# Kernel optimization log

Measured on AMD Instinct MI355X. Metric: run time of the kernel, lower is better.

## Reference

```python
import jax, jax.numpy as jnp
import numpy as np

DIM = 1024
NUM_HEADS = 16
HEAD_DIM = DIM // NUM_HEADS
SCALE = HEAD_DIM ** -0.5


def setup_inputs() -> dict:
    key = jax.random.key(0)
    k_x, k_wqkv, k_bqkv, k_wp, k_bp = jax.random.split(key, 5)
    B, C, D = 4, 1024, DIM
    x = jax.random.normal(k_x, (B, C, D), dtype=jnp.float32)
    # nn.Linear stores weight as (out, in); we keep (in, out) for x @ W
    w_qkv = jax.random.normal(k_wqkv, (D, 3 * D), dtype=jnp.float32) * (D ** -0.5)
    b_qkv = jax.random.normal(k_bqkv, (3 * D,), dtype=jnp.float32) * 0.02
    w_proj = jax.random.normal(k_wp, (D, D), dtype=jnp.float32) * (D ** -0.5)
    b_proj = jax.random.normal(k_bp, (D,), dtype=jnp.float32) * 0.02
    return {"x": x, "w_qkv": w_qkv, "b_qkv": b_qkv, "w_proj": w_proj, "b_proj": b_proj}


def reference(x, w_qkv, b_qkv, w_proj, b_proj):
    B, C, D = x.shape
    H, Hd = NUM_HEADS, HEAD_DIM
    qkv = x @ w_qkv + b_qkv                       # (B, C, 3D)
    qkv = qkv.reshape(B, C, 3, H, Hd)
    q = qkv[:, :, 0].transpose(0, 2, 1, 3)        # (B, H, C, Hd)
    k = qkv[:, :, 1].transpose(0, 2, 1, 3)
    v = qkv[:, :, 2].transpose(0, 2, 1, 3)
    attn = jnp.einsum('bhqd,bhkd->bhqk', q, k) * SCALE
    attn = jax.nn.softmax(attn, axis=-1)
    out = jnp.einsum('bhqk,bhkd->bhqd', attn, v)  # (B, H, C, Hd)
    out = out.transpose(0, 2, 1, 3).reshape(B, C, D)
    return out @ w_proj + b_proj
```

## Files before the change

### kernel.cpp

```cpp
#include <hip/hip_runtime.h>
#include <cstdint>

#define BB 4
#define CC 1024
#define DD 1024
#define HH 16
#define HD 64
#define NH3 3072

typedef __attribute__((ext_vector_type(8))) short short8;
typedef __attribute__((ext_vector_type(4))) float f32x4;

#define MFMA16(a, b, c) __builtin_amdgcn_mfma_f32_16x16x32_bf16(a, b, c, 0, 0, 0)
#define EXP2 __builtin_amdgcn_exp2f

__device__ __forceinline__ void glds16(const void* g, void* l) {
    __builtin_amdgcn_global_load_lds(
        (const __attribute__((address_space(1))) void*)g,
        (__attribute__((address_space(3))) void*)l, 16, 0, 0);
}

__device__ __forceinline__ ushort f2bf(float f) {
    union { float f; uint32_t u; } v; v.f = f;
    uint32_t r = v.u + 0x7FFF + ((v.u >> 16) & 1);
    return (ushort)(r >> 16);
}

__device__ __forceinline__ uint32_t pack2bf(float a, float b) {
    uint32_t ua = __float_as_uint(a), ub = __float_as_uint(b);
    ua += 0x7FFF + ((ua >> 16) & 1);
    ub += 0x7FFF + ((ub >> 16) & 1);
    return __builtin_amdgcn_perm(ua, ub, 0x03020706);
}

__global__ __launch_bounds__(256)
void prep_kernel(const float* __restrict__ x, ushort* __restrict__ xbf,
                 const float* __restrict__ wqkv, ushort* __restrict__ wqkvT,
                 const float* __restrict__ wprj, ushort* __restrict__ wprjT)
{
    __shared__ float Ts[64 * 65];
    const int blk = blockIdx.x;
    const int t = threadIdx.x;

    if (blk < 4096) {
        int i = blk * 256 + t;
        float4 v = ((const float4*)x)[i];
        ushort4 o;
        o.x = f2bf(v.x); o.y = f2bf(v.y); o.z = f2bf(v.z); o.w = f2bf(v.w);
        ((ushort4*)xbf)[i] = o;
        return;
    }

    const float* in; ushort* outp; int K, N, n0, k0;
    if (blk < 4864) {
        int bx = blk - 4096;
        in = wqkv; outp = wqkvT; K = DD; N = NH3;
        n0 = (bx % 48) * 64; k0 = (bx / 48) * 64;
    } else {
        int bx = blk - 4864;
        in = wprj; outp = wprjT; K = DD; N = DD;
        n0 = (bx % 16) * 64; k0 = (bx / 16) * 64;
    }
    #pragma unroll
    for (int i = 0; i < 16; ++i) {
        int idx = t + i * 256;
        int r = idx >> 6, c = idx & 63;
        Ts[r * 65 + c] = in[(size_t)(k0 + r) * N + n0 + c];
    }
    __syncthreads();
    #pragma unroll
    for (int i = 0; i < 16; ++i) {
        int idx = t + i * 256;
        int rr = idx >> 6, cc = idx & 63;
        outp[(size_t)(n0 + rr) * K + k0 + cc] = f2bf(Ts[cc * 65 + rr]);
    }
}

template<int MODE, int MT>
__global__ __launch_bounds__(256)
void gemm_bt(const ushort* __restrict__ A, const ushort* __restrict__ Bt,
             const float* __restrict__ bias, float* __restrict__ Cf,
             ushort* __restrict__ qb, ushort* __restrict__ kb, ushort* __restrict__ vtb,
             int M, int N, int K)
{
    constexpr int MI = MT / 32;
    __shared__ ushort As[2][MT * 32];
    __shared__ ushort Bs[2][128 * 32];

    const int tid = threadIdx.x;
    const int wid = tid >> 6, lane = tid & 63;
    const int quad = lane >> 4, l15 = lane & 15;
    const int m0 = blockIdx.y * MT, n0 = blockIdx.x * 128;
    const int wm = (wid >> 1) * (MT / 2), wn = (wid & 1) * 64;

    const int sr = lane >> 2;
    const int sc = lane & 3;

    const int ar0 = wid * (MT / 4) + sr;
    const int acg0 = sc ^ ((ar0 >> 1) & 3);
    const int acg1 = sc ^ (((ar0 + 16) >> 1) & 3);
    const ushort* Ar0 = A + (size_t)(m0 + ar0) * K + acg0 * 8;
    const ushort* Ar1 = A + (size_t)(m0 + ar0 + 16) * K + acg1 * 8;
    const int br0 = wid * 32 + sr;
    const int bcg0 = sc ^ ((br0 >> 1) & 3);
    const int bcg1 = sc ^ (((br0 + 16) >> 1) & 3);
    const ushort* Br0 = Bt + (size_t)(n0 + br0) * K + bcg0 * 8;
    const ushort* Br1 = Bt + (size_t)(n0 + br0 + 16) * K + bcg1 * 8;

    f32x4 acc[MI][4];
    #pragma unroll
    for (int i = 0; i < MI; ++i)
        #pragma unroll
        for (int j = 0; j < 4; ++j) acc[i][j] = (f32x4)(0.0f);

    glds16(Ar0, &As[0][(wid * (MT / 4)) * 32]);
    glds16(Br0, &Bs[0][(wid * 32) * 32]);
    if (MT == 128) glds16(Ar1, &As[0][(wid * 32 + 16) * 32]);
    glds16(Br1, &Bs[0][(wid * 32 + 16) * 32]);

    int buf = 0;
    for (int k0 = 0; k0 < K; k0 += 32) {
        __syncthreads();
        if (k0 + 32 < K) {
            const int kn = k0 + 32;
            glds16(Ar0 + kn, &As[buf ^ 1][(wid * (MT / 4)) * 32]);
            glds16(Br0 + kn, &Bs[buf ^ 1][(wid * 32) * 32]);
            if (MT == 128) glds16(Ar1 + kn, &As[buf ^ 1][(wid * 32 + 16) * 32]);
            glds16(Br1 + kn, &Bs[buf ^ 1][(wid * 32 + 16) * 32]);
        }

        short8 af[MI], bf[4];
        #pragma unroll
        for (int i = 0; i < MI; ++i) {
            int row = wm + i * 16 + l15;
            af[i] = *(const short8*)(&As[buf][row * 32 + (quad ^ ((row >> 1) & 3)) * 8]);
        }
        #pragma unroll
        for (int j = 0; j < 4; ++j) {
            int col = wn + j * 16 + l15;
            bf[j] = *(const short8*)(&Bs[buf][col * 32 + (quad ^ ((col >> 1) & 3)) * 8]);
        }
        #pragma unroll
        for (int i = 0; i < MI; ++i)
            #pragma unroll
            for (int j = 0; j < 4; ++j)
                acc[i][j] = MFMA16(af[i], bf[j], acc[i][j]);
        buf ^= 1;
    }

    if (MODE == 0) {
        #pragma unroll
        for (int i = 0; i < MI; ++i) {
            int row = m0 + wm + i * 16 + quad * 4;
            #pragma unroll
            for (int j = 0; j < 4; ++j) {
                int col = n0 + wn + j * 16 + l15;
                float bv = bias[col];
                #pragma unroll
                for (int r = 0; r < 4; ++r)
                    Cf[(size_t)(row + r) * N + col] = acc[i][j][r] + bv;
            }
        }
    } else {
        #pragma unroll
        for (int j = 0; j < 4; ++j) {
            int n = n0 + wn + j * 16 + l15;
            int three = n >> 10;
            int h = (n >> 6) & 15;
            int hd = n & 63;
            float scale = (three == 0) ? 0.1803368801f : 1.0f;
            float bv = bias[n];
            #pragma unroll
            for (int i = 0; i < MI; ++i) {
                int row = m0 + wm + i * 16 + quad * 4;
                #pragma unroll
                for (int r = 0; r < 4; ++r) {
                    int m = row + r;
                    int b = m >> 10, c = m & 1023;
                    ushort val = f2bf((acc[i][j][r] + bv) * scale);
                    if (three == 0)
                        qb[((size_t)((b * HH + h) * CC) + c) * HD + hd] = val;
                    else if (three == 1)
                        kb[((size_t)((b * HH + h) * CC) + c) * HD + hd] = val;
                    else
                        vtb[((size_t)((b * HH + h) * HD) + hd) * CC + c] = val;
                }
            }
        }
    }
}

__global__ __launch_bounds__(256)
void attn_mfma6(const ushort* __restrict__ qb, const ushort* __restrict__ kb,
                const ushort* __restrict__ vt, ushort* __restrict__ attnb)
{
    __shared__ ushort lds[2 * 4096 + 3 * 4096 + 2 * 9216];
    const uint K0 = 0, K1 = 4096;
    const uint V0 = 8192, V1 = 12288, V2 = 16384;
    const uint P0 = 20480, P1 = 29696;

    const int tid = threadIdx.x;
    const int wid = tid >> 6, lane = tid & 63;
    const int quad = lane >> 4, l15 = lane & 15;
    const int bh = blockIdx.x & 63;
    const int qt = blockIdx.x >> 6;
    const int q0 = qt * 128;
    const int b = bh >> 4, h = bh & 15;

    const ushort* Qp  = qb + ((size_t)bh * CC + q0) * HD;
    const ushort* Kp  = kb + (size_t)bh * CC * HD;
    const ushort* Vtp = vt + (size_t)bh * HD * CC;

    const int sr = lane >> 3;
    const int sc = lane & 7;

    short8 qf[2][2];
    #pragma unroll
    for (int q2 = 0; q2 < 2; ++q2) {
        int row = wid * 32 + q2 * 16 + l15;
        #pragma unroll
        for (int s = 0; s < 2; ++s)
            qf[q2][s] = *(const short8*)(Qp + (size_t)row * HD + (s * 4 + quad) * 8);
    }

    const int kr = wid * 16 + sr;
    const int cgA = sc ^ (kr & 7);
    const int cgB = sc ^ ((kr + 8) & 7);
    const ushort* Kr0 = Kp  + (size_t)kr * HD + cgA * 8;
    const ushort* Kr1 = Kp  + (size_t)(kr + 8) * HD + cgB * 8;
    const ushort* Vr0 = Vtp + (size_t)kr * CC + cgA * 8;
    const ushort* Vr1 = Vtp + (size_t)(kr + 8) * CC + cgB * 8;

    const uint stg0 = (wid * 16) * 64;
    const uint stg1 = (wid * 16 + 8) * 64;

    glds16(Kr0, lds + K0 + stg0);
    glds16(Kr1, lds + K0 + stg1);
    glds16(Vr0, lds + V0 + stg0);
    glds16(Vr1, lds + V0 + stg1);

    f32x4 oacc[2][4];
    #pragma unroll
    for (int q2 = 0; q2 < 2; ++q2)
        #pragma unroll
        for (int hb = 0; hb < 4; ++hb) oacc[q2][hb] = (f32x4)(0.0f);
    float lsum[2] = {0.0f, 0.0f};

    uint ksC = K0, ksN = K1;
    uint vsP = V2, vsC = V0, vsN = V1;
    uint psC = P0, psP = P1;

    for (int kt = 0; kt < 16; ++kt) {
        __syncthreads();
        if (kt < 15) {
            const int koff = (kt + 1) * 64;
            glds16(Kr0 + (size_t)koff * HD, lds + ksN + stg0);
            glds16(Kr1 + (size_t)koff * HD, lds + ksN + stg1);
            glds16(Vr0 + koff,              lds + vsN + stg0);
            glds16(Vr1 + koff,              lds + vsN + stg1);
        }

        if (kt > 0) {
            short8 vf[4][2];
            #pragma unroll
            for (int hb = 0; hb < 4; ++hb) {
                int hr = hb * 16 + l15;
                vf[hb][0] = *(const short8*)(lds + vsP + hr * 64 + ((quad ^ (hr & 7)) * 8));
                vf[hb][1] = *(const short8*)(lds + vsP + hr * 64 + (((4 + quad) ^ (hr & 7)) * 8));
            }
            #pragma unroll
            for (int q2 = 0; q2 < 2; ++q2) {
                int row = wid * 32 + q2 * 16 + l15;
                short8 pf0 = *(const short8*)(lds + psP + row * 72 + quad * 8);
                short8 pf1 = *(const short8*)(lds + psP + row * 72 + 32 + quad * 8);
                #pragma unroll
                for (int hb = 0; hb < 4; ++hb) {
                    oacc[q2][hb] = MFMA16(pf0, vf[hb][0], oacc[q2][hb]);
                    oacc[q2][hb] = MFMA16(pf1, vf[hb][1], oacc[q2][hb]);
                }
            }
        }

        #pragma unroll
        for (int kb2 = 0; kb2 < 4; ++kb2) {
            int krow = kb2 * 16 + l15;
            short8 kf0 = *(const short8*)(lds + ksC + krow * 64 + ((quad ^ (krow & 7)) * 8));
            short8 kf1 = *(const short8*)(lds + ksC + krow * 64 + (((4 + quad) ^ (krow & 7)) * 8));
            #pragma unroll
            for (int q2 = 0; q2 < 2; ++q2) {
                f32x4 st = (f32x4)(0.0f);
                st = MFMA16(kf0, qf[q2][0], st);
                st = MFMA16(kf1, qf[q2][1], st);
                float p0 = EXP2(st[0]);
                float p1 = EXP2(st[1]);
                float p2 = EXP2(st[2]);
                float p3 = EXP2(st[3]);
                lsum[q2] += (p0 + p1) + (p2 + p3);
                int row = wid * 32 + q2 * 16 + l15;
                *(uint2*)(lds + psC + row * 72 + kb2 * 16 + quad * 4) =
                    make_uint2(pack2bf(p0, p1), pack2bf(p2, p3));
            }
        }

        uint t = vsP; vsP = vsC; vsC = vsN; vsN = t;
        t = ksC; ksC = ksN; ksN = t;
        t = psP; psP = psC; psC = t;
    }

    {
        short8 vf[4][2];
        #pragma unroll
        for (int hb = 0; hb < 4; ++hb) {
            int hr = hb * 16 + l15;
            vf[hb][0] = *(const short8*)(lds + vsP + hr * 64 + ((quad ^ (hr & 7)) * 8));
            vf[hb][1] = *(const short8*)(lds + vsP + hr * 64 + (((4 + quad) ^ (hr & 7)) * 8));
        }
        #pragma unroll
        for (int q2 = 0; q2 < 2; ++q2) {
            int row = wid * 32 + q2 * 16 + l15;
            short8 pf0 = *(const short8*)(lds + psP + row * 72 + quad * 8);
            short8 pf1 = *(const short8*)(lds + psP + row * 72 + 32 + quad * 8);
            #pragma unroll
            for (int hb = 0; hb < 4; ++hb) {
                oacc[q2][hb] = MFMA16(pf0, vf[hb][0], oacc[q2][hb]);
                oacc[q2][hb] = MFMA16(pf1, vf[hb][1], oacc[q2][hb]);
            }
        }
    }

    #pragma unroll
    for (int q2 = 0; q2 < 2; ++q2) {
        lsum[q2] += __shfl_xor(lsum[q2], 16);
        lsum[q2] += __shfl_xor(lsum[q2], 32);
    }

    #pragma unroll
    for (int q2 = 0; q2 < 2; ++q2) {
        #pragma unroll
        for (int r = 0; r < 4; ++r) {
            float inv = 1.0f / __shfl(lsum[q2], (lane & 48) | (quad * 4 + r));
            int c = q0 + wid * 32 + q2 * 16 + quad * 4 + r;
            #pragma unroll
            for (int hb = 0; hb < 4; ++hb) {
                int d = h * 64 + hb * 16 + l15;
                attnb[((size_t)(b * CC + c)) * DD + d] = f2bf(oacc[q2][hb][r] * inv);
            }
        }
    }
}

extern "C" void kernel_launch(void* const* d_in, const int* in_sizes, int n_in,
                              void* d_out, int out_size, void* d_ws, size_t ws_size,
                              hipStream_t stream)
{
    (void)in_sizes; (void)n_in; (void)out_size; (void)ws_size;
    const float* x      = (const float*)d_in[0];
    const float* w_qkv  = (const float*)d_in[1];
    const float* b_qkv  = (const float*)d_in[2];
    const float* w_proj = (const float*)d_in[3];
    const float* b_proj = (const float*)d_in[4];
    float* out = (float*)d_out;

    ushort* p = (ushort*)d_ws;
    ushort* xbf   = p;  p += (size_t)4 * 1024 * 1024;
    ushort* wqkvT = p;  p += (size_t)3 * 1024 * 1024;
    ushort* wprjT = p;  p += (size_t)1 * 1024 * 1024;
    ushort* qbuf  = p;  p += (size_t)4 * 1024 * 1024;
    ushort* kbuf  = p;  p += (size_t)4 * 1024 * 1024;
    ushort* vtb   = p;  p += (size_t)4 * 1024 * 1024;
    ushort* attnb = p;  p += (size_t)4 * 1024 * 1024;

    prep_kernel<<<5120, 256, 0, stream>>>(x, xbf, w_qkv, wqkvT, w_proj, wprjT);

    gemm_bt<1, 128><<<dim3(NH3 / 128, (BB * CC) / 128), 256, 0, stream>>>(
        xbf, wqkvT, b_qkv, nullptr, qbuf, kbuf, vtb, BB * CC, NH3, DD);

    attn_mfma6<<<512, 256, 0, stream>>>(qbuf, kbuf, vtb, attnb);

    gemm_bt<0, 64><<<dim3(DD / 128, (BB * CC) / 64), 256, 0, stream>>>(
        attnb, wprjT, b_proj, out, nullptr, nullptr, nullptr, BB * CC, DD, DD);
}
```

Baseline: 177.8 us.

## Add 256x256 tiled QKV GEMM with 4-stage LDS pipeline

Replaces the 128x128 QKV projection GEMM with a dedicated kernel that uses 256x256 block tiles, 512 threads and a four-buffer direct global-to-LDS pipeline with swizzled layout. The larger tiles are meant to raise operand reuse and cut global and LDS traffic per MFMA. The trade-off is a grid of only 192 blocks, which leaves some CUs idle, plus higher register and LDS use per block.

```diff
diff --git a/kernel.cpp b/kernel.cpp
--- a/kernel.cpp
+++ b/kernel.cpp
@@ -190,6 +190,108 @@
     }
 }
 
+__global__ __launch_bounds__(512, 2)
+void gemm_qkv256(const ushort* __restrict__ A, const ushort* __restrict__ Bt,
+                 const float* __restrict__ bias,
+                 ushort* __restrict__ qb, ushort* __restrict__ kb,
+                 ushort* __restrict__ vtb)
+{
+    constexpr int K  = DD;
+    constexpr int KT = K / 32;
+    __shared__ ushort lds[4][16384];
+
+    const int tid = threadIdx.x;
+    const int wid = tid >> 6, lane = tid & 63;
+    const int quad = lane >> 4, l15 = lane & 15;
+    const int m0 = blockIdx.y * 256, n0 = blockIdx.x * 256;
+    const int wm = (wid >> 2) * 128, wn = (wid & 3) * 64;
+
+    const int sr = lane >> 2, sc = lane & 3;
+    const int ra = wid * 16 + sr;
+    const int cga = sc ^ ((ra >> 1) & 3);
+    const ushort* Ap0 = A  + (size_t)(m0 + ra) * K + cga * 8;
+    const ushort* Ap1 = Ap0 + (size_t)128 * K;
+    const ushort* Bp0 = Bt + (size_t)(n0 + ra) * K + cga * 8;
+    const ushort* Bp1 = Bp0 + (size_t)128 * K;
+    const int sA0 = (wid * 16) * 32;
+    const int sA1 = sA0 + 128 * 32;
+    const int sB0 = 8192 + sA0;
+    const int sB1 = 8192 + sA1;
+
+#define QSTAGE(kt) do { ushort* lb_ = &lds[(kt) & 3][0]; const int ko_ = (kt) * 32; \
+        glds16(Ap0 + ko_, lb_ + sA0); \
+        glds16(Ap1 + ko_, lb_ + sA1); \
+        glds16(Bp0 + ko_, lb_ + sB0); \
+        glds16(Bp1 + ko_, lb_ + sB1); } while (0)
+
+    f32x4 acc[8][4];
+    #pragma unroll
+    for (int i = 0; i < 8; ++i)
+        #pragma unroll
+        for (int j = 0; j < 4; ++j) acc[i][j] = (f32x4)(0.0f);
+
+    QSTAGE(0); QSTAGE(1); QSTAGE(2);
+
+#define QPHASE(kt, VMS, DOSTAGE) do { \
+        asm volatile("s_waitcnt " VMS "\n\ts_barrier" ::: "memory"); \
+        const ushort* ab_ = &lds[(kt) & 3][0]; \
+        short8 af_[8], bf_[4]; \
+        _Pragma("unroll") \
+        for (int i = 0; i < 8; ++i) { \
+            int row = wm + i * 16 + l15; \
+            af_[i] = *(const short8*)(ab_ + row * 32 + (quad ^ ((row >> 1) & 3)) * 8); } \
+        _Pragma("unroll") \
+        for (int j = 0; j < 4; ++j) { \
+            int col = wn + j * 16 + l15; \
+            bf_[j] = *(const short8*)(ab_ + 8192 + col * 32 + (quad ^ ((col >> 1) & 3)) * 8); } \
+        if (DOSTAGE) QSTAGE((kt) + 3); \
+        __builtin_amdgcn_s_setprio(1); \
+        _Pragma("unroll") \
+        for (int i = 0; i < 8; ++i) \
+            _Pragma("unroll") \
+            for (int j = 0; j < 4; ++j) \
+                acc[i][j] = MFMA16(af_[i], bf_[j], acc[i][j]); \
+        __builtin_amdgcn_s_setprio(0); \
+        __builtin_amdgcn_sched_barrier(0); \
+    } while (0)
+
+    #pragma unroll 4
+    for (int kt = 0; kt < KT - 4; ++kt)
+        QPHASE(kt, "vmcnt(8)", true);
+    QPHASE(KT - 4, "vmcnt(8)", true);
+    QPHASE(KT - 3, "vmcnt(8)", false);
+    QPHASE(KT - 2, "vmcnt(4)", false);
+    QPHASE(KT - 1, "vmcnt(0)", false);
+
+    #pragma unroll
+    for (int j = 0; j < 4; ++j) {
+        int n = n0 + wn + j * 16 + l15;
+        int three = n >> 10;
+        int h = (n >> 6) & 15;
+        int hd = n & 63;
+        float scale = (three == 0) ? 0.1803368801f : 1.0f;
+        float bv = bias[n];
+        #pragma unroll
+        for (int i = 0; i < 8; ++i) {
+            int row = m0 + wm + i * 16 + quad * 4;
+            #pragma unroll
+            for (int r = 0; r < 4; ++r) {
+                int m = row + r;
+                int b = m >> 10, c = m & 1023;
+                ushort val = f2bf((acc[i][j][r] + bv) * scale);
+                if (three == 0)
+                    qb[((size_t)((b * HH + h) * CC) + c) * HD + hd] = val;
+                else if (three == 1)
+                    kb[((size_t)((b * HH + h) * CC) + c) * HD + hd] = val;
+                else
+                    vtb[((size_t)((b * HH + h) * HD) + hd) * CC + c] = val;
+            }
+        }
+    }
+#undef QPHASE
+#undef QSTAGE
+}
+
 __global__ __launch_bounds__(256)
 void attn_mfma6(const ushort* __restrict__ qb, const ushort* __restrict__ kb,
                 const ushort* __restrict__ vt, ushort* __restrict__ attnb)
@@ -372,8 +474,8 @@
 
     prep_kernel<<<5120, 256, 0, stream>>>(x, xbf, w_qkv, wqkvT, w_proj, wprjT);
 
-    gemm_bt<1, 128><<<dim3(NH3 / 128, (BB * CC) / 128), 256, 0, stream>>>(
-        xbf, wqkvT, b_qkv, nullptr, qbuf, kbuf, vtb, BB * CC, NH3, DD);
+    gemm_qkv256<<<dim3(NH3 / 256, (BB * CC) / 256), 512, 0, stream>>>(
+        xbf, wqkvT, b_qkv, qbuf, kbuf, vtb);
 
     attn_mfma6<<<512, 256, 0, stream>>>(qbuf, kbuf, vtb, attnb);
 
```

Result: slower. 192.6 us (+8.4%).

## Triple-buffer GEMM LDS stages with partial vmcnt waits

Applied to the files above, without the earlier changes.

Changes the GEMM main loop from double to triple buffering in LDS. Two stages are prefetched and each iteration waits only for the older stage using a partial s_waitcnt vmcnt plus a barrier, in place of __syncthreads. This is meant to hide global-to-LDS load latency behind MFMA work. The cost is 50% more LDS per block, which could reduce occupancy. Correctness relies on the hand-counted outstanding load numbers.

```diff
diff --git a/kernel.cpp b/kernel.cpp
--- a/kernel.cpp
+++ b/kernel.cpp
@@ -84,8 +84,8 @@
              int M, int N, int K)
 {
     constexpr int MI = MT / 32;
-    __shared__ ushort As[2][MT * 32];
-    __shared__ ushort Bs[2][128 * 32];
+    __shared__ ushort As[3][MT * 32];
+    __shared__ ushort Bs[3][128 * 32];
 
     const int tid = threadIdx.x;
     const int wid = tid >> 6, lane = tid & 63;
@@ -113,40 +113,50 @@
         #pragma unroll
         for (int j = 0; j < 4; ++j) acc[i][j] = (f32x4)(0.0f);
 
-    glds16(Ar0, &As[0][(wid * (MT / 4)) * 32]);
-    glds16(Br0, &Bs[0][(wid * 32) * 32]);
-    if (MT == 128) glds16(Ar1, &As[0][(wid * 32 + 16) * 32]);
-    glds16(Br1, &Bs[0][(wid * 32 + 16) * 32]);
-
-    int buf = 0;
+#define GSTAGE(kn, bidx) do { \
+        glds16(Ar0 + (kn), &As[bidx][(wid * (MT / 4)) * 32]); \
+        glds16(Br0 + (kn), &Bs[bidx][(wid * 32) * 32]); \
+        if (MT == 128) glds16(Ar1 + (kn), &As[bidx][(wid * 32 + 16) * 32]); \
+        glds16(Br1 + (kn), &Bs[bidx][(wid * 32 + 16) * 32]); } while (0)
+
+    GSTAGE(0, 0);
+    GSTAGE(32, 1);
+
+    int cur = 0;
     for (int k0 = 0; k0 < K; k0 += 32) {
-        __syncthreads();
         if (k0 + 32 < K) {
-            const int kn = k0 + 32;
-            glds16(Ar0 + kn, &As[buf ^ 1][(wid * (MT / 4)) * 32]);
-            glds16(Br0 + kn, &Bs[buf ^ 1][(wid * 32) * 32]);
-            if (MT == 128) glds16(Ar1 + kn, &As[buf ^ 1][(wid * 32 + 16) * 32]);
-            glds16(Br1 + kn, &Bs[buf ^ 1][(wid * 32 + 16) * 32]);
+            if (MT == 128)
+                asm volatile("s_waitcnt vmcnt(4)\n\ts_barrier" ::: "memory");
+            else
+                asm volatile("s_waitcnt vmcnt(3)\n\ts_barrier" ::: "memory");
+        } else {
+            asm volatile("s_waitcnt vmcnt(0)\n\ts_barrier" ::: "memory");
+        }
+        if (k0 + 64 < K) {
+            const int nb = (cur >= 1) ? cur - 1 : 2;
+            GSTAGE(k0 + 64, nb);
         }
 
         short8 af[MI], bf[4];
         #pragma unroll
         for (int i = 0; i < MI; ++i) {
             int row = wm + i * 16 + l15;
-            af[i] = *(const short8*)(&As[buf][row * 32 + (quad ^ ((row >> 1) & 3)) * 8]);
+            af[i] = *(const short8*)(&As[cur][row * 32 + (quad ^ ((row >> 1) & 3)) * 8]);
         }
         #pragma unroll
         for (int j = 0; j < 4; ++j) {
             int col = wn + j * 16 + l15;
-            bf[j] = *(const short8*)(&Bs[buf][col * 32 + (quad ^ ((col >> 1) & 3)) * 8]);
+            bf[j] = *(const short8*)(&Bs[cur][col * 32 + (quad ^ ((col >> 1) & 3)) * 8]);
         }
         #pragma unroll
         for (int i = 0; i < MI; ++i)
             #pragma unroll
             for (int j = 0; j < 4; ++j)
                 acc[i][j] = MFMA16(af[i], bf[j], acc[i][j]);
-        buf ^= 1;
-    }
+
+        cur = (cur == 2) ? 0 : cur + 1;
+    }
+#undef GSTAGE
 
     if (MODE == 0) {
         #pragma unroll
```

Result: no change. 176.4 us (-0.7%).
